# Performance work log

Hardware: AMD Instinct MI355X
Metric: run time of the kernel (lower is better)

Reference implementation:

```python
import jax, jax.numpy as jnp
import numpy as np

N_NODES = 100000
N_EDGES = 1600000
DIM_IN, DIM_H, DIM_OUT = 500, 64, 8


def setup_inputs() -> dict:
    key = jax.random.key(0)
    k_x, k_e, k_w1, k_w2 = jax.random.split(key, 4)
    x = jax.random.normal(k_x, (N_NODES, DIM_IN), dtype=jnp.float32)
    edge_index = jax.random.randint(k_e, (2, N_EDGES), 0, N_NODES, dtype=jnp.int32)
    # Glorot-ish init for linear weights, zero bias (PyG GCNConv default)
    W1 = jax.random.normal(k_w1, (DIM_IN, DIM_H), dtype=jnp.float32) * (1.0 / np.sqrt(DIM_IN))
    b1 = jnp.zeros((DIM_H,), dtype=jnp.float32)
    W2 = jax.random.normal(k_w2, (DIM_H, DIM_OUT), dtype=jnp.float32) * (1.0 / np.sqrt(DIM_H))
    b2 = jnp.zeros((DIM_OUT,), dtype=jnp.float32)
    return {"x": x, "edge_index": edge_index, "W1": W1, "b1": b1, "W2": W2, "b2": b2}


def _gcn_conv(h, W, b, src, dst, edge_norm, num_nodes):
    """GCNConv: out = D^{-1/2}(A+I)D^{-1/2} (h W) + b, via gather/scatter over edges."""
    hw = h @ W                                  # [N, d_out] dense transform
    msg = hw[src] * edge_norm[:, None]          # [E+N, d_out] gather + scale
    agg = jax.ops.segment_sum(msg, dst, num_segments=num_nodes)  # scatter-add
    return agg + b


def reference(x, edge_index, W1, b1, W2, b2):
    num_nodes = x.shape[0]
    # Add self-loops (PyG GCNConv default: add_self_loops=True)
    loops = jnp.arange(num_nodes, dtype=edge_index.dtype)
    src = jnp.concatenate([edge_index[0], loops])
    dst = jnp.concatenate([edge_index[1], loops])
    # Symmetric normalization from in-degree of loop-augmented graph
    deg = jax.ops.segment_sum(jnp.ones_like(dst, dtype=x.dtype), dst,
                              num_segments=num_nodes)
    dinv = jnp.where(deg > 0, jax.lax.rsqrt(deg), 0.0)
    edge_norm = dinv[src] * dinv[dst]           # [E+N]
    # Eval-mode forward (dropout is identity when not training)
    h = jax.nn.relu(_gcn_conv(x, W1, b1, src, dst, edge_norm, num_nodes))
    h = _gcn_conv(h, W2, b2, src, dst, edge_norm, num_nodes)
    return jax.nn.log_softmax(h, axis=1)
```

## Files before the change

kernel.cpp:

```cpp
#include <hip/hip_runtime.h>
#include <stdint.h>

#define NN 100000
#define NE 1600000
#define DIN 500
#define DH 64
#define DOUT 8
#define KP 512
#define MAXDEG 64
#define LDSW 132

#define FILL_EPT 4
#define FILL_PASSES 16
#define FILL_RS ((NN + FILL_PASSES - 1) / FILL_PASSES)

typedef __attribute__((ext_vector_type(8))) short short8;
typedef __attribute__((ext_vector_type(4))) float f32x4;
typedef unsigned short ushort_t;

static __device__ __forceinline__ ushort_t f2bf(float f) {
  union { float f; uint32_t u; } v; v.f = f;
  uint32_t u = v.u;
  return (ushort_t)((u + 0x7FFFu + ((u >> 16) & 1u)) >> 16);
}
static __device__ __forceinline__ float bf2f(ushort_t h) {
  union { uint32_t u; float f; } v; v.u = ((uint32_t)h) << 16;
  return v.f;
}

__global__ __launch_bounds__(256) void k_fill(const int* __restrict__ ei,
                                              int* __restrict__ cursor,
                                              int* __restrict__ colsrc) {
  int t = blockIdx.x * 256 + threadIdx.x;
  const int T = gridDim.x * 256;
  int s[FILL_EPT], d[FILL_EPT];
#pragma unroll
  for (int k = 0; k < FILL_EPT; ++k) {
    int id = t + k * T;
    s[k] = 0; d[k] = -1;
    if (id < NE) { s[k] = ei[id]; d[k] = ei[NE + id]; }
    else if (id < NE + NN) { s[k] = id - NE; d[k] = s[k]; }
  }
#pragma unroll 1
  for (int p = 0; p < FILL_PASSES; ++p) {
    int lo = p * FILL_RS;
    int hi = lo + FILL_RS;
#pragma unroll
    for (int k = 0; k < FILL_EPT; ++k) {
      bool act = (d[k] >= lo) && (d[k] < hi);
      if (__any(act)) {
        if (act) {
          int pos = atomicAdd(&cursor[d[k]], 1);
          if (pos < MAXDEG) colsrc[d[k] * MAXDEG + pos] = s[k];
        }
      }
    }
  }
}

__global__ __launch_bounds__(256) void k_dinv(const int* __restrict__ cursor,
                                              float* __restrict__ dinv) {
  int v = blockIdx.x * 256 + threadIdx.x;
  if (v >= NN) return;
  dinv[v] = 1.0f / sqrtf((float)cursor[v]);
}

__global__ __launch_bounds__(256) void k_w1cvt(const float* __restrict__ W1,
                                               ushort_t* __restrict__ bt) {
  int id = blockIdx.x * 256 + threadIdx.x;
  if (id >= DH * KP * 2) return;
  int i = id & 7, lane = (id >> 3) & 63, h = (id >> 9) & 1;
  int off = (id >> 10) & 3, kkg = id >> 12;
  int r = lane & 15, g = lane >> 4;
  int col = off * 16 + r;
  int k = kkg * 32 + g * 8 + i;
  float v = (k < DIN) ? W1[k * DH + col] : 0.0f;
  ushort_t hi = f2bf(v);
  bt[id] = h ? f2bf(v - bf2f(hi)) : hi;
}

__global__ __launch_bounds__(256) void k_gemm1(const float* __restrict__ x,
                                               const ushort_t* __restrict__ bt,
                                               ushort_t* __restrict__ hwb) {
  __shared__ float lds[2][64 * LDSW];
  int tid = threadIdx.x;
  int lane = tid & 63, w = tid >> 6;
  int r = lane & 15, g = lane >> 4;
  int row0 = blockIdx.x * 64;

  f32x4 st[8];
  const f32x4 z4 = {0, 0, 0, 0};

  auto loadRegs = [&](int ch) {
#pragma unroll
    for (int j = 0; j < 8; ++j) {
      int idx = j * 256 + tid;
      int lr = idx >> 5;
      int q = idx & 31;
      int kq = ch * 32 + q;
      int grow = row0 + lr;
      if (kq < 125 && grow < NN)
        st[j] = __builtin_nontemporal_load((const f32x4*)(x + (size_t)grow * DIN + kq * 4));
      else
        st[j] = z4;
    }
  };
  auto writeLDS = [&](int b) {
#pragma unroll
    for (int j = 0; j < 8; ++j) {
      int idx = j * 256 + tid;
      int lr = idx >> 5;
      int q = idx & 31;
      *(f32x4*)(&lds[b][lr * LDSW + q * 4]) = st[j];
    }
  };

  f32x4 acc0 = {0,0,0,0}, acc1 = {0,0,0,0}, acc2 = {0,0,0,0}, acc3 = {0,0,0,0};

  loadRegs(0);
  writeLDS(0);
#pragma unroll 1
  for (int ch = 0; ch < 4; ++ch) {
    __syncthreads();
    if (ch < 3) loadRegs(ch + 1);
    __builtin_amdgcn_sched_barrier(0);
#pragma unroll
    for (int kk = 0; kk < 4; ++kk) {
      const float* lp = &lds[ch & 1][(w * 16 + r) * LDSW + kk * 32 + g * 8];
      f32x4 v0 = *(const f32x4*)lp;
      f32x4 v1 = *(const f32x4*)(lp + 4);
      float a[8] = {v0.x, v0.y, v0.z, v0.w, v1.x, v1.y, v1.z, v1.w};
      short8 ah, al;
#pragma unroll
      for (int i = 0; i < 8; ++i) {
        ushort_t hi = f2bf(a[i]);
        ah[i] = (short)hi;
        al[i] = (short)f2bf(a[i] - bf2f(hi));
      }
      int kkg = ch * 4 + kk;
      const ushort_t* bph = bt + (size_t)(kkg * 4 * 2) * 512 + lane * 8;
#define TILE(T, OFF)                                                            \
      {                                                                         \
        short8 bhf = *(const short8*)(bph + (OFF) * 2 * 512);                   \
        short8 blf = *(const short8*)(bph + ((OFF) * 2 + 1) * 512);             \
        T = __builtin_amdgcn_mfma_f32_16x16x32_bf16(ah, bhf, T, 0, 0, 0);       \
        T = __builtin_amdgcn_mfma_f32_16x16x32_bf16(al, bhf, T, 0, 0, 0);       \
        T = __builtin_amdgcn_mfma_f32_16x16x32_bf16(ah, blf, T, 0, 0, 0);       \
      }
      TILE(acc0, 0) TILE(acc1, 1) TILE(acc2, 2) TILE(acc3, 3)
#undef TILE
    }
    __builtin_amdgcn_sched_barrier(0);
    if (ch < 3) writeLDS((ch + 1) & 1);
  }
  int wrow0 = row0 + w * 16;
#pragma unroll
  for (int i = 0; i < 4; ++i) {
    int orow = wrow0 + g * 4 + i;
    if (orow < NN) {
      ushort_t* o = hwb + (size_t)orow * DH + r;
      o[0]  = f2bf(acc0[i]);
      o[16] = f2bf(acc1[i]);
      o[32] = f2bf(acc2[i]);
      o[48] = f2bf(acc3[i]);
    }
  }
}

__global__ __launch_bounds__(256) void k_agg1(const ushort_t* __restrict__ hwb,
                                              const int* __restrict__ colsrc,
                                              const int* __restrict__ cnt,
                                              const float* __restrict__ dinv,
                                              const float* __restrict__ b1,
                                              const float* __restrict__ W2,
                                              float* __restrict__ hw2) {
  int lane = threadIdx.x & 63;
  int v = blockIdx.x * 4 + (threadIdx.x >> 6);
  if (v >= NN) return;
  int c = cnt[v]; if (c > MAXDEG) c = MAXDEG;
  float dv = dinv[v];
  const int* cl = colsrc + v * MAXDEG;
  int si = cl[lane];
  bool act = lane < c;
  if (!act) si = 0;
  float nrmv = act ? dinv[si] * dv : 0.0f;
  float acc = 0.0f;
  for (int i0 = 0; i0 < c; i0 += 16) {
    float val[16];
#pragma unroll
    for (int j = 0; j < 16; ++j) {
      int s = __builtin_amdgcn_readlane(si, i0 + j);
      val[j] = bf2f(hwb[(size_t)s * DH + lane]);
    }
#pragma unroll
    for (int j = 0; j < 16; ++j) {
      float nrm = __uint_as_float(__builtin_amdgcn_readlane(__float_as_uint(nrmv), i0 + j));
      acc = fmaf(val[j], nrm, acc);
    }
  }
  float h = acc + b1[lane];
  h = h > 0.0f ? h : 0.0f;
  const float* w2r = W2 + lane * DOUT;
  float p0 = h * w2r[0], p1 = h * w2r[1], p2 = h * w2r[2], p3 = h * w2r[3];
  float p4 = h * w2r[4], p5 = h * w2r[5], p6 = h * w2r[6], p7 = h * w2r[7];
#pragma unroll
  for (int off = 32; off > 0; off >>= 1) {
    p0 += __shfl_xor(p0, off); p1 += __shfl_xor(p1, off);
    p2 += __shfl_xor(p2, off); p3 += __shfl_xor(p3, off);
    p4 += __shfl_xor(p4, off); p5 += __shfl_xor(p5, off);
    p6 += __shfl_xor(p6, off); p7 += __shfl_xor(p7, off);
  }
  if (lane == 0) {
    float4 q0 = {p0, p1, p2, p3}, q1 = {p4, p5, p6, p7};
    *(float4*)(hw2 + (size_t)v * DOUT)     = q0;
    *(float4*)(hw2 + (size_t)v * DOUT + 4) = q1;
  }
}

__global__ __launch_bounds__(256) void k_agg2(const float* __restrict__ hw2,
                                              const int* __restrict__ colsrc,
                                              const int* __restrict__ cnt,
                                              const float* __restrict__ dinv,
                                              const float* __restrict__ b2,
                                              float* __restrict__ out) {
  int lane = threadIdx.x & 63;
  int v = blockIdx.x * 4 + (threadIdx.x >> 6);
  if (v >= NN) return;
  int e = lane >> 3, f = lane & 7;
  int c = cnt[v]; if (c > MAXDEG) c = MAXDEG;
  float dv = dinv[v];
  const int* cl = colsrc + v * MAXDEG;
  float acc = 0.0f;
  for (int i0 = 0; i0 < c; i0 += 8) {
    int i = i0 + e;
    bool a2 = i < c;
    int s = a2 ? cl[i] : 0;
    float nrm = a2 ? dinv[s] * dv : 0.0f;
    float val = hw2[(size_t)s * DOUT + f] * nrm;
    val += __shfl_xor(val, 8);
    val += __shfl_xor(val, 16);
    val += __shfl_xor(val, 32);
    acc += val;
  }
  acc += b2[f];
  float m = acc;
  m = fmaxf(m, __shfl_xor(m, 1));
  m = fmaxf(m, __shfl_xor(m, 2));
  m = fmaxf(m, __shfl_xor(m, 4));
  float ex = expf(acc - m);
  float sum = ex;
  sum += __shfl_xor(sum, 1);
  sum += __shfl_xor(sum, 2);
  sum += __shfl_xor(sum, 4);
  float ls = m + logf(sum);
  if (e == 0) out[(size_t)v * DOUT + f] = acc - ls;
}

extern "C" void kernel_launch(void* const* d_in, const int* in_sizes, int n_in,
                              void* d_out, int out_size, void* d_ws, size_t ws_size,
                              hipStream_t stream) {
  const float* x  = (const float*)d_in[0];
  const int*   ei = (const int*)d_in[1];
  const float* W1 = (const float*)d_in[2];
  const float* b1 = (const float*)d_in[3];
  const float* W2 = (const float*)d_in[4];
  const float* b2 = (const float*)d_in[5];
  float* out = (float*)d_out;

  char* w = (char*)d_ws;
  size_t off = 0;
  auto alloc = [&](size_t bytes) {
    char* p = w + off;
    off += (bytes + 255) & ~(size_t)255;
    return (void*)p;
  };
  int*      cursor = (int*)alloc((size_t)NN * 4);
  float*    dinv   = (float*)alloc((size_t)NN * 4);
  ushort_t* bt     = (ushort_t*)alloc((size_t)DH * KP * 2 * 2);
  int*      colsrc = (int*)alloc((size_t)NN * MAXDEG * 4);
  ushort_t* hwb    = (ushort_t*)alloc((size_t)NN * DH * 2);
  float*    hw2    = (float*)alloc((size_t)NN * DOUT * 4);

  hipMemsetAsync(cursor, 0, (size_t)NN * 4, stream);
  int fill_blocks = (NE + NN + 256 * FILL_EPT - 1) / (256 * FILL_EPT);
  k_fill<<<fill_blocks, 256, 0, stream>>>(ei, cursor, colsrc);
  k_dinv<<<(NN + 255) / 256, 256, 0, stream>>>(cursor, dinv);
  k_w1cvt<<<(DH * KP * 2 + 255) / 256, 256, 0, stream>>>(W1, bt);
  k_gemm1<<<(NN + 63) / 64, 256, 0, stream>>>(x, bt, hwb);
  k_agg1<<<(NN + 3) / 4, 256, 0, stream>>>(hwb, colsrc, cursor, dinv, b1, W2, hw2);
  k_agg2<<<(NN + 3) / 4, 256, 0, stream>>>(hw2, colsrc, cursor, dinv, b2, out);
}
```

Baseline: 279.4 us.

## Stage GEMM1 input tiles with direct global-to-LDS loads and XOR swizzle

Replaces the register-staged copy of x chunks (global load into VGPRs, then an LDS write) with `global_load_lds` 16-byte transfers that write straight into the double-buffered LDS tile. The padded LDS row stride is replaced by an XOR swizzle on the 16-byte column index to avoid bank conflicts. Out-of-range columns and rows are clamped rather than zero-filled; this relies on the zero-padded W1 rows to cancel the extra K values and on the output-row bound check. It frees staging registers and the LDS store instructions, and moves the barrier to the end of each chunk. It gives up the nontemporal load hint, and prefetching now depends on the LDS DMA being waited on before each barrier.

```diff
diff --git a/kernel.cpp b/kernel.cpp
--- a/kernel.cpp
+++ b/kernel.cpp
@@ -8,7 +8,6 @@
 #define DOUT 8
 #define KP 512
 #define MAXDEG 64
-#define LDSW 132
 
 #define FILL_EPT 4
 #define FILL_PASSES 16
@@ -26,6 +25,11 @@
 static __device__ __forceinline__ float bf2f(ushort_t h) {
   union { uint32_t u; float f; } v; v.u = ((uint32_t)h) << 16;
   return v.f;
+}
+
+static __device__ __forceinline__ void gload16(const void* g, void* l) {
+  __builtin_amdgcn_global_load_lds((const __attribute__((address_space(1))) uint32_t*)g,
+                                   (__attribute__((address_space(3))) uint32_t*)l, 16, 0, 0);
 }
 
 __global__ __launch_bounds__(256) void k_fill(const int* __restrict__ ei,
@@ -82,53 +86,43 @@
 __global__ __launch_bounds__(256) void k_gemm1(const float* __restrict__ x,
                                                const ushort_t* __restrict__ bt,
                                                ushort_t* __restrict__ hwb) {
-  __shared__ float lds[2][64 * LDSW];
+  __shared__ float lds[2][64 * 128];
   int tid = threadIdx.x;
   int lane = tid & 63, w = tid >> 6;
   int r = lane & 15, g = lane >> 4;
   int row0 = blockIdx.x * 64;
 
-  f32x4 st[8];
-  const f32x4 z4 = {0, 0, 0, 0};
-
-  auto loadRegs = [&](int ch) {
+  auto stage = [&](int ch, int b) {
+    float* base = &lds[b][0];
 #pragma unroll
     for (int j = 0; j < 8; ++j) {
       int idx = j * 256 + tid;
-      int lr = idx >> 5;
-      int q = idx & 31;
-      int kq = ch * 32 + q;
-      int grow = row0 + lr;
-      if (kq < 125 && grow < NN)
-        st[j] = __builtin_nontemporal_load((const f32x4*)(x + (size_t)grow * DIN + kq * 4));
-      else
-        st[j] = z4;
+      int row = idx >> 5;
+      int q   = idx & 31;
+      int qd  = q ^ (row & 7);
+      int kq  = ch * 32 + qd;
+      if (kq > 124) kq = 124;
+      int grow = row0 + row;
+      if (grow >= NN) grow = NN - 1;
+      gload16(x + (size_t)grow * DIN + kq * 4, base + idx * 4);
     }
   };
-  auto writeLDS = [&](int b) {
-#pragma unroll
-    for (int j = 0; j < 8; ++j) {
-      int idx = j * 256 + tid;
-      int lr = idx >> 5;
-      int q = idx & 31;
-      *(f32x4*)(&lds[b][lr * LDSW + q * 4]) = st[j];
-    }
-  };
 
   f32x4 acc0 = {0,0,0,0}, acc1 = {0,0,0,0}, acc2 = {0,0,0,0}, acc3 = {0,0,0,0};
-
-  loadRegs(0);
-  writeLDS(0);
+  int rowl = w * 16 + r;
+  int sw = rowl & 7;
+
+  stage(0, 0);
+  __syncthreads();
 #pragma unroll 1
   for (int ch = 0; ch < 4; ++ch) {
-    __syncthreads();
-    if (ch < 3) loadRegs(ch + 1);
+    if (ch < 3) stage(ch + 1, (ch + 1) & 1);
     __builtin_amdgcn_sched_barrier(0);
 #pragma unroll
     for (int kk = 0; kk < 4; ++kk) {
-      const float* lp = &lds[ch & 1][(w * 16 + r) * LDSW + kk * 32 + g * 8];
-      f32x4 v0 = *(const f32x4*)lp;
-      f32x4 v1 = *(const f32x4*)(lp + 4);
+      int q0 = kk * 8 + g * 2;
+      f32x4 v0 = *(const f32x4*)(&lds[ch & 1][rowl * 128 + ((q0)     ^ sw) * 4]);
+      f32x4 v1 = *(const f32x4*)(&lds[ch & 1][rowl * 128 + ((q0 + 1) ^ sw) * 4]);
       float a[8] = {v0.x, v0.y, v0.z, v0.w, v1.x, v1.y, v1.z, v1.w};
       short8 ah, al;
 #pragma unroll
@@ -150,8 +144,7 @@
       TILE(acc0, 0) TILE(acc1, 1) TILE(acc2, 2) TILE(acc3, 3)
 #undef TILE
     }
-    __builtin_amdgcn_sched_barrier(0);
-    if (ch < 3) writeLDS((ch + 1) & 1);
+    __syncthreads();
   }
   int wrow0 = row0 + w * 16;
 #pragma unroll
```

Measured after the change: 286.7 us. 2.6% more time.
